# Optimization experiments

Hardware: AMD Instinct MI355X
Metric: run time of the kernel (lower is better)

## Reference

```python
import jax, jax.numpy as jnp
import numpy as np

N_NODES = 100000
N_EDGES = 1600000
N_GRAPHS = 512


def gcn_conv(x, src, dst, W, b, n_nodes):
    """PyG GCNConv: add self-loops, symmetric norm, linear, scatter-add, bias."""
    h = x @ W.T                                   # [N, out]
    ones = jnp.ones(src.shape[0], dtype=x.dtype)
    deg = jax.ops.segment_sum(ones, dst, num_segments=n_nodes)   # in-degree incl. self-loops
    dinv = jnp.where(deg > 0, jax.lax.rsqrt(deg), 0.0)
    norm = dinv[src] * dinv[dst]                  # [E+N]
    msg = h[src] * norm[:, None]                  # gather + scale
    out = jax.ops.segment_sum(msg, dst, num_segments=n_nodes)
    return out + b


def setup_inputs() -> dict:
    key = jax.random.key(0)
    ks = jax.random.split(key, 8)
    x = jax.random.normal(ks[0], (N_NODES, 2), dtype=jnp.float32)
    edge_index = jax.random.randint(ks[1], (2, N_EDGES), 0, N_NODES, dtype=jnp.int64)
    batch = jnp.sort(jax.random.randint(ks[2], (N_NODES,), 0, N_GRAPHS, dtype=jnp.int64))
    def glorot(k, shape):
        lim = jnp.sqrt(6.0 / (shape[0] + shape[1])).astype(jnp.float32)
        return jax.random.uniform(k, shape, jnp.float32, -lim, lim)
    return {
        "x": x, "edge_index": edge_index, "batch": batch,
        "W1": glorot(ks[3], (32, 2)),  "b1": jnp.zeros(32, jnp.float32),
        "W2": glorot(ks[4], (64, 32)), "b2": jnp.zeros(64, jnp.float32),
        "W3": glorot(ks[5], (32, 64)), "b3": jnp.zeros(32, jnp.float32),
        "Wfc": glorot(ks[6], (1, 32)), "bfc": jnp.zeros(1, jnp.float32),
    }


def reference(x, edge_index, batch, W1, b1, W2, b2, W3, b3, Wfc, bfc):
    n = x.shape[0]
    loop = jnp.arange(n, dtype=edge_index.dtype)
    src = jnp.concatenate([edge_index[0], loop])  # self-loops appended once
    dst = jnp.concatenate([edge_index[1], loop])

    h = jax.nn.relu(gcn_conv(x, src, dst, W1, b1, n))   # dropout = identity (eval)
    h = jax.nn.relu(gcn_conv(h, src, dst, W2, b2, n))
    h = jax.nn.relu(gcn_conv(h, src, dst, W3, b3, n))

    # global_mean_pool over graph ids
    sums = jax.ops.segment_sum(h, batch, num_segments=N_GRAPHS)
    cnts = jax.ops.segment_sum(jnp.ones((n,), h.dtype), batch, num_segments=N_GRAPHS)
    pooled = sums / jnp.maximum(cnts, 1.0)[:, None]     # [G, 32]
    return pooled @ Wfc.T + bfc                         # [G, 1]
```

## Files before the change

kernel.cpp:

```cpp
#include <hip/hip_runtime.h>
#include <hip/hip_fp16.h>


static constexpr int TPB = 256;
static constexpr int NB1 = 256;
static constexpr int NB_SCAN = 256;
static constexpr int P2CAP = 6144;

__global__ void p1_hist_gptr_kernel(const int* __restrict__ dst, int* __restrict__ hist,
                                    int E, int chunk, int shift, int B,
                                    const int* __restrict__ batch, int* __restrict__ gstart,
                                    int n, int G) {
  int b = blockIdx.x, t = threadIdx.x;
  if (b >= NB1) {
    int i = (b - NB1) * TPB + t;
    if (i >= n) return;
    int bb = batch[i];
    int bp = (i == 0) ? -1 : batch[i - 1];
    for (int g = bp + 1; g <= bb; ++g) gstart[g] = i;
    if (i == n - 1)
      for (int g = bb + 1; g <= G; ++g) gstart[g] = n;
    return;
  }
  __shared__ int h[1024];
  for (int i = t; i < B; i += TPB) h[i] = 0;
  __syncthreads();
  int lo = b * chunk, hi = min(lo + chunk, E);
  for (int e = lo + t; e < hi; e += TPB) atomicAdd(&h[dst[e] >> shift], 1);
  __syncthreads();
  for (int i = t; i < B; i += TPB) hist[i * NB1 + b] = h[i];
}

__global__ void scan_partial_kernel(const int* __restrict__ a, int* __restrict__ bsum,
                                    int n, int seg) {
  int b = blockIdx.x, t = threadIdx.x;
  int lo = b * seg, hi = min(lo + seg, n);
  int acc = 0;
  for (int i = lo + t; i < hi; i += TPB) acc += a[i];
  __shared__ int red[TPB];
  red[t] = acc;
  __syncthreads();
  for (int st = TPB / 2; st > 0; st >>= 1) {
    if (t < st) red[t] += red[t + st];
    __syncthreads();
  }
  if (t == 0) bsum[b] = red[0];
}

__global__ void scan_emit_kernel(int* __restrict__ a, const int* __restrict__ bsum,
                                 int n, int seg) {
  int b = blockIdx.x, t = threadIdx.x;
  int lo = b * seg, hi = min(lo + seg, n);
  __shared__ int cs[TPB];
  __shared__ int s_run;
  cs[t] = (t < b) ? bsum[t] : 0;
  __syncthreads();
  for (int st = TPB / 2; st > 0; st >>= 1) {
    if (t < st) cs[t] += cs[t + st];
    __syncthreads();
  }
  if (t == 0) s_run = cs[0];
  __syncthreads();
  for (int base = lo; base < hi; base += TPB) {
    int i = base + t;
    int v = (i < hi) ? a[i] : 0;
    cs[t] = v;
    __syncthreads();
    for (int off = 1; off < TPB; off <<= 1) {
      int u = (t >= off) ? cs[t - off] : 0;
      __syncthreads();
      cs[t] += u;
      __syncthreads();
    }
    if (i < hi) a[i] = s_run + cs[t] - v;
    __syncthreads();
    if (t == 0) s_run += cs[TPB - 1];
    __syncthreads();
  }
}

__global__ void p1_scatter_kernel(const int* __restrict__ src, const int* __restrict__ dst,
                                  const int* __restrict__ hist, unsigned int* __restrict__ epk,
                                  int E, int chunk, int shift, int srcbits, int B) {
  __shared__ int cur[1024];
  int b = blockIdx.x, t = threadIdx.x;
  for (int i = t; i < B; i += TPB) cur[i] = hist[i * NB1 + b];
  __syncthreads();
  int lo = b * chunk, hi = min(lo + chunk, E);
  int span1 = (1 << shift) - 1;
  for (int e = lo + t; e < hi; e += TPB) {
    int d = dst[e];
    int pos = atomicAdd(&cur[d >> shift], 1);
    epk[pos] = ((unsigned int)(d & span1) << srcbits) | (unsigned int)src[e];
  }
}

__global__ __launch_bounds__(TPB) void p2_sort_kernel(
    const unsigned int* __restrict__ epk, const int* __restrict__ hist,
    const float2* __restrict__ x2,
    int* __restrict__ rowptr, float* __restrict__ dinv, float2* __restrict__ u0,
    int* __restrict__ esrc, int N, int E, int shift, int srcbits, int B) {
  int bkt = blockIdx.x, t = threadIdx.x;
  int span = 1 << shift;
  int nb = bkt << shift;
  int bstart = hist[bkt * NB1];
  int bend = (bkt + 1 < B) ? hist[(bkt + 1) * NB1] : E;
  int bsize = bend - bstart;
  __shared__ int cnt[256];
  __shared__ int ex[256];
  __shared__ int ldata[P2CAP];
  __shared__ int lsrc[P2CAP];
  bool stage = (bsize <= P2CAP);
  if (t < span) cnt[t] = 0;
  __syncthreads();
  if (stage) {
    for (int i = t; i < bsize; i += TPB) ldata[i] = (int)epk[bstart + i];
    __syncthreads();
    for (int i = t; i < bsize; i += TPB)
      atomicAdd(&cnt[((unsigned int)ldata[i]) >> srcbits], 1);
  } else {
    for (int e = bstart + t; e < bend; e += TPB) atomicAdd(&cnt[epk[e] >> srcbits], 1);
  }
  __syncthreads();
  int v = (t < span) ? cnt[t] : 0;
  ex[t] = v;
  __syncthreads();
  for (int off = 1; off < 256; off <<= 1) {
    int u = (t >= off) ? ex[t - off] : 0;
    __syncthreads();
    ex[t] += u;
    __syncthreads();
  }
  int excl = ex[t] - v;
  int node = nb + t;
  if (t < span && node < N) {
    rowptr[node] = bstart + excl;
    float dv = rsqrtf((float)v + 1.0f);
    dinv[node] = dv;
    float2 xv = x2[node];
    u0[node] = make_float2(xv.x * dv, xv.y * dv);
  }
  if (bkt == 0 && t == 0) rowptr[N] = E;
  __syncthreads();
  if (t < span) cnt[t] = stage ? excl : bstart + excl;
  __syncthreads();
  if (stage) {
    for (int i = t; i < bsize; i += TPB) {
      int p = ldata[i];
      int pos = atomicAdd(&cnt[((unsigned int)p) >> srcbits], 1);
      lsrc[pos] = p;
    }
    __syncthreads();
    for (int i = t; i < bsize; i += TPB) esrc[bstart + i] = lsrc[i];
  } else {
    for (int e = bstart + t; e < bend; e += TPB) {
      unsigned int p = epk[e];
      int pos = atomicAdd(&cnt[p >> srcbits], 1);
      esrc[pos] = (int)p;
    }
  }
}

__global__ void layer1_kernel(const float2* __restrict__ u0, const int* __restrict__ rowptr,
                              const int* __restrict__ esrc, const float* __restrict__ W1,
                              const float* __restrict__ b1, const float* __restrict__ dinv,
                              __half* __restrict__ u1_16, int n, int srcbits) {
  int tid = blockIdx.x * blockDim.x + threadIdx.x;
  int i = tid >> 2, split = tid & 3;
  if (i >= n) return;
  unsigned int smask = (1u << srcbits) - 1u;
  float ax = 0.f, ay = 0.f;
  if (split == 0) {
    float2 s = u0[i];
    ax = s.x; ay = s.y;
  }
  int r0 = rowptr[i], r1 = rowptr[i + 1];
  int e = r0 + split;
  while (e + 4 < r1) {
    int s0 = esrc[e] & smask, s1 = esrc[e + 4] & smask;
    float2 v0 = u0[s0];
    float2 v1 = u0[s1];
    ax += v0.x + v1.x;
    ay += v0.y + v1.y;
    e += 8;
  }
  if (e < r1) {
    float2 v = u0[esrc[e] & smask];
    ax += v.x; ay += v.y;
  }
  ax += __shfl_xor(ax, 1, 64); ay += __shfl_xor(ay, 1, 64);
  ax += __shfl_xor(ax, 2, 64); ay += __shfl_xor(ay, 2, 64);
  float di = dinv[i];
  int f0 = split * 8;
  union { float4 f4[1]; __half h[8]; } oh;
#pragma unroll
  for (int k = 0; k < 8; ++k) {
    int f = f0 + k;
    float hv = fmaxf(di * (W1[f * 2 + 0] * ax + W1[f * 2 + 1] * ay) + b1[f], 0.f);
    oh.h[k] = __float2half(di * hv);
  }
  *(float4*)&u1_16[(size_t)i * 32 + f0] = oh.f4[0];
}

template <bool EPI>
__global__ __launch_bounds__(TPB) void gpush_kernel(
    const float4* __restrict__ a16, const int* __restrict__ rowptr,
    const int* __restrict__ esrc, const float* __restrict__ dinv,
    const float* __restrict__ b, float4* __restrict__ out16, int n, int srcbits) {
  constexpr int SA = 34;
  __shared__ float accum[64 * SA];
  int t = threadIdx.x;
  int base = blockIdx.x * 64;
  unsigned int smask = (1u << srcbits) - 1u;
  int nl = t >> 2, q = t & 3;
  int node = base + nl;
  {
    union { float4 f4; __half2 h2[4]; } u;
    u.f4 = (node < n) ? a16[(size_t)node * 4 + q] : make_float4(0.f, 0.f, 0.f, 0.f);
    float* dp = &accum[nl * SA + q * 8];
#pragma unroll
    for (int k = 0; k < 4; ++k) *(float2*)&dp[2 * k] = __half22float2(u.h2[k]);
  }
  __syncthreads();
  int e0 = rowptr[base];
  int e1 = rowptr[min(base + 64, n)];
  int ne = e1 - e0;
  int nIter = (ne + 63) >> 6;
  int my0 = nl * nIter;
  int myn = min(my0 + nIter, ne);
  float acc[8] = {0.f, 0.f, 0.f, 0.f, 0.f, 0.f, 0.f, 0.f};
  int cur = -1;
  for (int ei = my0; ei < myn; ++ei) {
    unsigned int p = (unsigned int)esrc[e0 + ei];
    union { float4 f4; __half2 h2[4]; } u;
    u.f4 = a16[(size_t)(p & smask) * 4 + q];
    int dl = (int)(p >> srcbits) & 63;
    if (dl != cur) {
      if (cur >= 0) {
        float* ap = &accum[cur * SA + q * 8];
#pragma unroll
        for (int k = 0; k < 8; ++k) unsafeAtomicAdd(&ap[k], acc[k]);
      }
      cur = dl;
#pragma unroll
      for (int k = 0; k < 8; ++k) acc[k] = 0.f;
    }
    float2 a0 = __half22float2(u.h2[0]);
    float2 a1 = __half22float2(u.h2[1]);
    float2 a2 = __half22float2(u.h2[2]);
    float2 a3 = __half22float2(u.h2[3]);
    acc[0] += a0.x; acc[1] += a0.y; acc[2] += a1.x; acc[3] += a1.y;
    acc[4] += a2.x; acc[5] += a2.y; acc[6] += a3.x; acc[7] += a3.y;
  }
  if (cur >= 0) {
    float* ap = &accum[cur * SA + q * 8];
#pragma unroll
    for (int k = 0; k < 8; ++k) unsafeAtomicAdd(&ap[k], acc[k]);
  }
  __syncthreads();
  if (node >= n) return;
  float o8[8];
  {
    const float* sp = &accum[nl * SA + q * 8];
#pragma unroll
    for (int k = 0; k < 4; ++k) {
      float2 v = *(const float2*)&sp[2 * k];
      o8[2 * k + 0] = v.x;
      o8[2 * k + 1] = v.y;
    }
  }
  if (EPI) {
    float di = dinv[node];
    const float4 bv0 = ((const float4*)b)[2 * q];
    const float4 bv1 = ((const float4*)b)[2 * q + 1];
    o8[0] = fmaxf(di * o8[0] + bv0.x, 0.f);
    o8[1] = fmaxf(di * o8[1] + bv0.y, 0.f);
    o8[2] = fmaxf(di * o8[2] + bv0.z, 0.f);
    o8[3] = fmaxf(di * o8[3] + bv0.w, 0.f);
    o8[4] = fmaxf(di * o8[4] + bv1.x, 0.f);
    o8[5] = fmaxf(di * o8[5] + bv1.y, 0.f);
    o8[6] = fmaxf(di * o8[6] + bv1.z, 0.f);
    o8[7] = fmaxf(di * o8[7] + bv1.w, 0.f);
  }
  union { float4 f4; __half2 h2[4]; } o;
  o.h2[0] = __floats2half2_rn(o8[0], o8[1]);
  o.h2[1] = __floats2half2_rn(o8[2], o8[3]);
  o.h2[2] = __floats2half2_rn(o8[4], o8[5]);
  o.h2[3] = __floats2half2_rn(o8[6], o8[7]);
  out16[(size_t)node * 4 + q] = o.f4;
}

__global__ __launch_bounds__(TPB) void t2t3_kernel(
    const float4* __restrict__ U1h, const float* __restrict__ W2, const float* __restrict__ b2,
    const float* __restrict__ W3, const float* __restrict__ dinv,
    __half* __restrict__ g3_16, int n) {
  constexpr int SN = 136;
  __shared__ float U1l[32 * SN];
  __shared__ float h2l[64 * SN];
  __shared__ float W2l[32 * 68];
  __shared__ float W3l[64 * 36];
  __shared__ float dil[128];
  int t = threadIdx.x;
  int base = blockIdx.x * 128;
  for (int idx = t; idx < 2048; idx += TPB) {
    int k = idx >> 5, j = idx & 31;
    W2l[j * 68 + k] = W2[idx];
  }
  for (int idx = t; idx < 2048; idx += TPB) {
    int k = idx >> 6, j = idx & 63;
    W3l[j * 36 + k] = W3[idx];
  }
  if (t < 128) dil[t] = (base + t < n) ? dinv[base + t] : 0.f;
  for (int it = 0; it < 2; ++it) {
    int idx = it * 256 + t;
    int nl = idx >> 2, j0 = (idx & 3) * 8;
    int node = base + nl;
    union { float4 f4; __half2 h2[4]; } u;
    u.f4 = (node < n) ? U1h[(size_t)node * 4 + (idx & 3)]
                      : make_float4(0.f, 0.f, 0.f, 0.f);
#pragma unroll
    for (int k = 0; k < 4; ++k) {
      float2 p = __half22float2(u.h2[k]);
      U1l[(j0 + 2 * k + 0) * SN + nl] = p.x;
      U1l[(j0 + 2 * k + 1) * SN + nl] = p.y;
    }
  }
  __syncthreads();
  {
    int a = t & 15, bb = t >> 4;
    int n0 = a * 8, k0 = bb * 4;
    float acc[4][8];
#pragma unroll
    for (int kk = 0; kk < 4; ++kk)
#pragma unroll
      for (int nn = 0; nn < 8; ++nn) acc[kk][nn] = 0.f;
#pragma unroll 8
    for (int j = 0; j < 32; ++j) {
      float4 ua = *(const float4*)&U1l[j * SN + n0];
      float4 ub = *(const float4*)&U1l[j * SN + n0 + 4];
      float4 w = *(const float4*)&W2l[j * 68 + k0];
      float un[8] = {ua.x, ua.y, ua.z, ua.w, ub.x, ub.y, ub.z, ub.w};
      float wk[4] = {w.x, w.y, w.z, w.w};
#pragma unroll
      for (int kk = 0; kk < 4; ++kk)
#pragma unroll
        for (int nn = 0; nn < 8; ++nn) acc[kk][nn] += un[nn] * wk[kk];
    }
    float4 bv = ((const float4*)b2)[bb];
    float bk[4] = {bv.x, bv.y, bv.z, bv.w};
#pragma unroll
    for (int kk = 0; kk < 4; ++kk) {
      float o[8];
#pragma unroll
      for (int nn = 0; nn < 8; ++nn)
        o[nn] = fmaxf(dil[n0 + nn] * acc[kk][nn] + bk[kk], 0.f);
      *(float4*)&h2l[(k0 + kk) * SN + n0] = make_float4(o[0], o[1], o[2], o[3]);
      *(float4*)&h2l[(k0 + kk) * SN + n0 + 4] = make_float4(o[4], o[5], o[6], o[7]);
    }
  }
  __syncthreads();
  {
    int a = t & 15, bb = t >> 4;
    int n0 = a * 8, k0 = bb * 2;
    float acc[2][8];
#pragma unroll
    for (int kk = 0; kk < 2; ++kk)
#pragma unroll
      for (int nn = 0; nn < 8; ++nn) acc[kk][nn] = 0.f;
#pragma unroll 8
    for (int j = 0; j < 64; ++j) {
      float4 ua = *(const float4*)&h2l[j * SN + n0];
      float4 ub = *(const float4*)&h2l[j * SN + n0 + 4];
      float w0 = W3l[j * 36 + k0];
      float w1 = W3l[j * 36 + k0 + 1];
      float un[8] = {ua.x, ua.y, ua.z, ua.w, ub.x, ub.y, ub.z, ub.w};
#pragma unroll
      for (int nn = 0; nn < 8; ++nn) {
        acc[0][nn] += un[nn] * w0;
        acc[1][nn] += un[nn] * w1;
      }
    }
#pragma unroll
    for (int nn = 0; nn < 8; ++nn) {
      int node = base + n0 + nn;
      if (node < n) {
        float di = dil[n0 + nn];
        __half2 hv = __floats2half2_rn(di * acc[0][nn], di * acc[1][nn]);
        *(__half2*)&g3_16[(size_t)node * 32 + k0] = hv;
      }
    }
  }
}

__global__ void poolfc_kernel(const __half2* __restrict__ h3, const int* __restrict__ gstart,
                              const float* __restrict__ Wfc, const float* __restrict__ bfc,
                              float* __restrict__ out) {
  int gi = blockIdx.x;
  int s = gstart[gi], e = gstart[gi + 1];
  int t = threadIdx.x;
  int nl = t >> 4, f2 = t & 15;
  float ax = 0.f, ay = 0.f;
  for (int i = s + nl; i < e; i += 16) {
    float2 v = __half22float2(h3[(size_t)i * 16 + f2]);
    ax += v.x; ay += v.y;
  }
  __shared__ float redx[256], redy[256];
  redx[t] = ax; redy[t] = ay;
  __syncthreads();
  for (int st = 128; st >= 16; st >>= 1) {
    if (t < st) { redx[t] += redx[t + st]; redy[t] += redy[t + st]; }
    __syncthreads();
  }
  if (t < 16) {
    float cnt = fmaxf((float)(e - s), 1.f);
    float v = (redx[t] / cnt) * Wfc[2 * t] + (redy[t] / cnt) * Wfc[2 * t + 1];
    for (int o = 8; o; o >>= 1) v += __shfl_down(v, o, 16);
    if (t == 0) out[gi] = v + bfc[0];
  }
}

extern "C" void kernel_launch(void* const* d_in, const int* in_sizes, int n_in,
                              void* d_out, int out_size, void* d_ws, size_t ws_size,
                              hipStream_t stream) {
  const float* x     = (const float*)d_in[0];
  const int*   ei    = (const int*)d_in[1];
  const int*   batch = (const int*)d_in[2];
  const float* W1    = (const float*)d_in[3];
  const float* b1    = (const float*)d_in[4];
  const float* W2    = (const float*)d_in[5];
  const float* b2    = (const float*)d_in[6];
  const float* W3    = (const float*)d_in[7];
  const float* b3    = (const float*)d_in[8];
  const float* Wfc   = (const float*)d_in[9];
  const float* bfc   = (const float*)d_in[10];
  float* out = (float*)d_out;

  const int N = in_sizes[0] / 2;
  const int E = in_sizes[1] / 2;
  const int G = out_size;
  const int* src = ei;
  const int* dst = ei + E;

  int shift = 8;
  while ((((N + (1 << shift) - 1) >> shift)) > 1024) ++shift;
  const int B = (N + (1 << shift) - 1) >> shift;
  const int srcbits = 32 - shift;
  const int chunkE = (E + NB1 - 1) / NB1;
  const int M = B * NB1;
  const int segM = (M + NB_SCAN - 1) / NB_SCAN;

  char* ws = (char*)d_ws;
  size_t off = 0;
  auto alloc = [&](size_t bytes) -> char* {
    char* p = ws + off;
    off += (bytes + 255) & ~(size_t)255;
    return p;
  };
  float*        dinv   = (float*)alloc((size_t)N * 4);
  int*          rowptr = (int*)alloc((size_t)(N + 1) * 4);
  int*          esrc   = (int*)alloc((size_t)E * 4);
  int*          gstart = (int*)alloc((size_t)(G + 1) * 4);
  int*          hist   = (int*)alloc((size_t)M * 4);
  int*          bsum   = (int*)alloc((size_t)NB_SCAN * 4);
  unsigned int* epk    = (unsigned int*)alloc((size_t)E * 4);
  float2*       u0     = (float2*)alloc((size_t)N * 8);
  __half*       u1_16  = (__half*)alloc((size_t)N * 32 * 2);
  __half*       U1h    = (__half*)alloc((size_t)N * 32 * 2);
  __half*       g3_16  = (__half*)alloc((size_t)N * 32 * 2);
  __half*       hA16   = (__half*)alloc((size_t)N * 32 * 2);

  const int gptrBlocks = (N + TPB - 1) / TPB;
  p1_hist_gptr_kernel<<<NB1 + gptrBlocks, TPB, 0, stream>>>(dst, hist, E, chunkE, shift, B,
                                                            batch, gstart, N, G);
  scan_partial_kernel<<<NB_SCAN, TPB, 0, stream>>>(hist, bsum, M, segM);
  scan_emit_kernel<<<NB_SCAN, TPB, 0, stream>>>(hist, bsum, M, segM);
  p1_scatter_kernel<<<NB1, TPB, 0, stream>>>(src, dst, hist, epk, E, chunkE, shift, srcbits, B);
  p2_sort_kernel<<<B, TPB, 0, stream>>>(epk, hist, (const float2*)x, rowptr, dinv, u0, esrc,
                                        N, E, shift, srcbits, B);

  layer1_kernel<<<((size_t)N * 4 + TPB - 1) / TPB, TPB, 0, stream>>>(
      u0, rowptr, esrc, W1, b1, dinv, u1_16, N, srcbits);

  const int gpushBlocks = (N + 63) / 64;
  gpush_kernel<false><<<gpushBlocks, TPB, 0, stream>>>(
      (const float4*)u1_16, rowptr, esrc, dinv, b2, (float4*)U1h, N, srcbits);
  t2t3_kernel<<<(N + 127) / 128, TPB, 0, stream>>>(
      (const float4*)U1h, W2, b2, W3, dinv, g3_16, N);

  gpush_kernel<true><<<gpushBlocks, TPB, 0, stream>>>(
      (const float4*)g3_16, rowptr, esrc, dinv, b3, (float4*)hA16, N, srcbits);

  poolfc_kernel<<<G, 256, 0, stream>>>((const __half2*)hA16, gstart, Wfc, bfc, out);
}
```

Before: 256.1 us.

## Halve nodes per gpush block and unroll edge gathers for more loads in flight

The gpush kernel now handles 32 destination nodes per block instead of 64, so each of the 64 edge slots covers fewer edges, and the block count doubles. Its edge loop is unrolled by four, issuing four gathers before accumulating to raise memory-level parallelism. The layer1 gather loop is likewise unrolled from two to four loads per iteration. The trade-off is more blocks, each with repeated setup and a shorter edge range, plus extra register pressure from the unrolling. Masking the destination-local index with GPN-1 relies on the packed sort key keeping the local id within 32.

```diff
diff --git a/kernel.cpp b/kernel.cpp
--- a/kernel.cpp
+++ b/kernel.cpp
@@ -6,6 +6,7 @@
 static constexpr int NB1 = 256;
 static constexpr int NB_SCAN = 256;
 static constexpr int P2CAP = 6144;
+static constexpr int GPN = 32;
 
 __global__ void p1_hist_gptr_kernel(const int* __restrict__ dst, int* __restrict__ hist,
                                     int E, int chunk, int shift, int B,
@@ -176,17 +177,21 @@
   }
   int r0 = rowptr[i], r1 = rowptr[i + 1];
   int e = r0 + split;
-  while (e + 4 < r1) {
+  while (e + 12 < r1) {
     int s0 = esrc[e] & smask, s1 = esrc[e + 4] & smask;
+    int s2 = esrc[e + 8] & smask, s3 = esrc[e + 12] & smask;
     float2 v0 = u0[s0];
     float2 v1 = u0[s1];
-    ax += v0.x + v1.x;
-    ay += v0.y + v1.y;
-    e += 8;
-  }
-  if (e < r1) {
+    float2 v2 = u0[s2];
+    float2 v3 = u0[s3];
+    ax += v0.x + v1.x + v2.x + v3.x;
+    ay += v0.y + v1.y + v2.y + v3.y;
+    e += 16;
+  }
+  while (e < r1) {
     float2 v = u0[esrc[e] & smask];
     ax += v.x; ay += v.y;
+    e += 4;
   }
   ax += __shfl_xor(ax, 1, 64); ay += __shfl_xor(ay, 1, 64);
   ax += __shfl_xor(ax, 2, 64); ay += __shfl_xor(ay, 2, 64);
@@ -208,13 +213,14 @@
     const int* __restrict__ esrc, const float* __restrict__ dinv,
     const float* __restrict__ b, float4* __restrict__ out16, int n, int srcbits) {
   constexpr int SA = 34;
-  __shared__ float accum[64 * SA];
+  __shared__ float accum[GPN * SA];
   int t = threadIdx.x;
-  int base = blockIdx.x * 64;
+  int base = blockIdx.x * GPN;
   unsigned int smask = (1u << srcbits) - 1u;
-  int nl = t >> 2, q = t & 3;
-  int node = base + nl;
-  {
+  int q = t & 3;
+  if (t < GPN * 4) {
+    int nl = t >> 2;
+    int node = base + nl;
     union { float4 f4; __half2 h2[4]; } u;
     u.f4 = (node < n) ? a16[(size_t)node * 4 + q] : make_float4(0.f, 0.f, 0.f, 0.f);
     float* dp = &accum[nl * SA + q * 8];
@@ -223,41 +229,59 @@
   }
   __syncthreads();
   int e0 = rowptr[base];
-  int e1 = rowptr[min(base + 64, n)];
+  int e1 = rowptr[min(base + GPN, n)];
   int ne = e1 - e0;
+  int slot = t >> 2;
   int nIter = (ne + 63) >> 6;
-  int my0 = nl * nIter;
-  int myn = min(my0 + nIter, ne);
+  int e = e0 + slot * nIter;
+  int eend = min(e + nIter, e1);
   float acc[8] = {0.f, 0.f, 0.f, 0.f, 0.f, 0.f, 0.f, 0.f};
   int cur = -1;
-  for (int ei = my0; ei < myn; ++ei) {
-    unsigned int p = (unsigned int)esrc[e0 + ei];
+  auto flushf = [&]() {
+    float* ap = &accum[cur * SA + q * 8];
+#pragma unroll
+    for (int k = 0; k < 8; ++k) unsafeAtomicAdd(&ap[k], acc[k]);
+  };
+  auto proc = [&](unsigned int p, float4 f) {
+    int dl = (int)(p >> srcbits) & (GPN - 1);
+    if (dl != cur) {
+      if (cur >= 0) flushf();
+      cur = dl;
+#pragma unroll
+      for (int k = 0; k < 8; ++k) acc[k] = 0.f;
+    }
     union { float4 f4; __half2 h2[4]; } u;
-    u.f4 = a16[(size_t)(p & smask) * 4 + q];
-    int dl = (int)(p >> srcbits) & 63;
-    if (dl != cur) {
-      if (cur >= 0) {
-        float* ap = &accum[cur * SA + q * 8];
-#pragma unroll
-        for (int k = 0; k < 8; ++k) unsafeAtomicAdd(&ap[k], acc[k]);
-      }
-      cur = dl;
-#pragma unroll
-      for (int k = 0; k < 8; ++k) acc[k] = 0.f;
-    }
+    u.f4 = f;
     float2 a0 = __half22float2(u.h2[0]);
     float2 a1 = __half22float2(u.h2[1]);
     float2 a2 = __half22float2(u.h2[2]);
     float2 a3 = __half22float2(u.h2[3]);
     acc[0] += a0.x; acc[1] += a0.y; acc[2] += a1.x; acc[3] += a1.y;
     acc[4] += a2.x; acc[5] += a2.y; acc[6] += a3.x; acc[7] += a3.y;
-  }
-  if (cur >= 0) {
-    float* ap = &accum[cur * SA + q * 8];
-#pragma unroll
-    for (int k = 0; k < 8; ++k) unsafeAtomicAdd(&ap[k], acc[k]);
-  }
-  __syncthreads();
+  };
+  while (e + 4 <= eend) {
+    unsigned int p0 = (unsigned int)esrc[e];
+    unsigned int p1 = (unsigned int)esrc[e + 1];
+    unsigned int p2 = (unsigned int)esrc[e + 2];
+    unsigned int p3 = (unsigned int)esrc[e + 3];
+    float4 f0 = a16[(size_t)(p0 & smask) * 4 + q];
+    float4 f1 = a16[(size_t)(p1 & smask) * 4 + q];
+    float4 f2 = a16[(size_t)(p2 & smask) * 4 + q];
+    float4 f3 = a16[(size_t)(p3 & smask) * 4 + q];
+    proc(p0, f0); proc(p1, f1); proc(p2, f2); proc(p3, f3);
+    e += 4;
+  }
+  while (e < eend) {
+    unsigned int p = (unsigned int)esrc[e];
+    float4 f = a16[(size_t)(p & smask) * 4 + q];
+    proc(p, f);
+    ++e;
+  }
+  if (cur >= 0) flushf();
+  __syncthreads();
+  if (t >= GPN * 4) return;
+  int nl = t >> 2;
+  int node = base + nl;
   if (node >= n) return;
   float o8[8];
   {
@@ -481,7 +505,7 @@
   layer1_kernel<<<((size_t)N * 4 + TPB - 1) / TPB, TPB, 0, stream>>>(
       u0, rowptr, esrc, W1, b1, dinv, u1_16, N, srcbits);
 
-  const int gpushBlocks = (N + 63) / 64;
+  const int gpushBlocks = (N + GPN - 1) / GPN;
   gpush_kernel<false><<<gpushBlocks, TPB, 0, stream>>>(
       (const float4*)u1_16, rowptr, esrc, dinv, b2, (float4*)U1h, N, srcbits);
   t2t3_kernel<<<(N + 127) / 128, TPB, 0, stream>>>(
```

New measurement: 276.1 us. +7.8%, slower.
